# Kernel tuning notes

Measured on AMD Instinct MI355X. Metric: run time of the kernel, lower is better.

## Reference

```python
import jax, jax.numpy as jnp
import numpy as np

N = 50000
NEG_SLOPE = 0.2  # PyG GATConv default negative_slope


def gat_conv(x, src, dst, W, a_src, a_dst, b, num_nodes):
    """PyG-style GATConv (concat=True, add_self_loops handled by caller).
    x: [N, Fin], src/dst: [E'] (self-loops included), W: [Fin, H*C],
    a_src/a_dst: [H, C], b: [H*C].
    """
    H, C = a_src.shape
    h = (x @ W).reshape(num_nodes, H, C)                      # [N, H, C]
    alpha_src = jnp.einsum('nhc,hc->nh', h, a_src)            # [N, H]
    alpha_dst = jnp.einsum('nhc,hc->nh', h, a_dst)            # [N, H]
    e = jax.nn.leaky_relu(alpha_src[src] + alpha_dst[dst], NEG_SLOPE)  # [E', H]
    # segment softmax over edges grouped by destination node
    m = jax.ops.segment_max(e, dst, num_segments=num_nodes)   # [N, H]
    m = jnp.where(jnp.isfinite(m), m, 0.0)
    ex = jnp.exp(e - m[dst])                                  # [E', H]
    denom = jax.ops.segment_sum(ex, dst, num_segments=num_nodes)
    alpha = ex / (denom[dst] + 1e-16)                          # [E', H]
    # weighted scatter-sum of source features to destinations
    out = jax.ops.segment_sum(alpha[:, :, None] * h[src], dst, num_segments=num_nodes)
    return out.reshape(num_nodes, H * C) + b


def setup_inputs() -> dict:
    key = jax.random.key(0)
    ks = jax.random.split(key, 10)
    Fin, Hid, Out, Hds = 128, 32, 64, 4
    E = 800000
    x = jax.random.normal(ks[0], (N, Fin), dtype=jnp.float32)
    edge_index = jax.random.randint(ks[1], (2, E), 0, N, dtype=jnp.int64)
    s1 = (1.0 / np.sqrt(Fin)).astype(np.float32) if isinstance(np.sqrt(Fin), np.ndarray) else np.float32(1.0 / np.sqrt(Fin))
    s2 = np.float32(1.0 / np.sqrt(Hid * Hds))
    return {
        'x': x,
        'edge_index': edge_index,
        'W1': jax.random.normal(ks[2], (Fin, Hds * Hid), dtype=jnp.float32) * s1,
        'att_src1': jax.random.normal(ks[3], (Hds, Hid), dtype=jnp.float32) * 0.1,
        'att_dst1': jax.random.normal(ks[4], (Hds, Hid), dtype=jnp.float32) * 0.1,
        'b1': jnp.zeros((Hds * Hid,), dtype=jnp.float32),
        'W2': jax.random.normal(ks[5], (Hds * Hid, Out), dtype=jnp.float32) * s2,
        'att_src2': jax.random.normal(ks[6], (1, Out), dtype=jnp.float32) * 0.1,
        'att_dst2': jax.random.normal(ks[7], (1, Out), dtype=jnp.float32) * 0.1,
        'b2': jnp.zeros((Out,), dtype=jnp.float32),
    }


def reference(x, edge_index, W1, att_src1, att_dst1, b1, W2, att_src2, att_dst2, b2):
    num_nodes = x.shape[0]
    loop = jnp.arange(num_nodes, dtype=edge_index.dtype)
    src = jnp.concatenate([edge_index[0], loop])  # add self-loops (PyG default)
    dst = jnp.concatenate([edge_index[1], loop])
    h = gat_conv(x, src, dst, W1, att_src1, att_dst1, b1, num_nodes)
    h = jax.nn.relu(h)
    out = gat_conv(h, src, dst, W2, att_src2, att_dst2, b2, num_nodes)
    return out
```

## Files before the change

kernel.cpp:

```cpp
#include <hip/hip_runtime.h>
#include <hip/hip_fp16.h>

#define NN 50000
#define EE 800000
#define ELL (EE + NN)
#define NSLICE 8
#define SLICE_W (NN / NSLICE)
#define LCAP 131072
#define LCNT_STRIDE 16
#define BUCK_TILE 4096

__device__ __forceinline__ int edge_at(const void* ei, int is64, long long idx) {
  if (is64) return (int)((const long long*)ei)[idx];
  return ((const int*)ei)[idx];
}

__device__ __forceinline__ float leaky(float x) { return x > 0.f ? x : 0.2f * x; }


__global__ void __launch_bounds__(256) zero_detect_kernel(int* __restrict__ p, int n,
                                                          const unsigned* __restrict__ ei_words,
                                                          int* __restrict__ flag) {
  if (blockIdx.x == 0 && threadIdx.x == 0) {
    unsigned acc = 0;
    for (int i = 1; i < 64; i += 2) acc |= ei_words[i];
    *flag = (acc == 0u) ? 1 : 0;
  }
  int stride = gridDim.x * blockDim.x;
  for (int i = blockIdx.x * blockDim.x + threadIdx.x; i < n; i += stride) p[i] = 0;
}


__global__ void __launch_bounds__(256) bucket_kernel(const void* __restrict__ ei,
                                                     const int* __restrict__ flag,
                                                     unsigned* __restrict__ lists,
                                                     int* __restrict__ lcnt) {
  __shared__ int hist[NSLICE];
  __shared__ int base[NSLICE];
  __shared__ int cur[NSLICE];
  int is64 = *flag;
  int t = threadIdx.x;
  if (t < NSLICE) hist[t] = 0;
  __syncthreads();
  long long i0 = (long long)blockIdx.x * BUCK_TILE;
  unsigned pk[16];
  int sl[16];
  #pragma unroll
  for (int j = 0; j < 16; ++j) {
    long long i = i0 + t + j * 256;
    int s = -1, d = -1;
    if (i < EE) {
      s = edge_at(ei, is64, i);
      d = edge_at(ei, is64, (long long)EE + i);
    } else if (i < ELL) {
      s = d = (int)(i - EE);
    }
    if ((unsigned)s < (unsigned)NN && (unsigned)d < (unsigned)NN) {
      sl[j] = d / SLICE_W;
      pk[j] = (unsigned)s | ((unsigned)d << 16);
      atomicAdd(&hist[sl[j]], 1);
    } else {
      sl[j] = -1;
    }
  }
  __syncthreads();
  if (t < NSLICE) {
    base[t] = atomicAdd(&lcnt[t * LCNT_STRIDE], hist[t]);
    cur[t] = 0;
  }
  __syncthreads();
  #pragma unroll
  for (int j = 0; j < 16; ++j) {
    if (sl[j] >= 0) {
      int pos = base[sl[j]] + atomicAdd(&cur[sl[j]], 1);
      if (pos < LCAP) lists[(sl[j] << 17) + pos] = pk[j];
    }
  }
}


__global__ void __launch_bounds__(256) count_kernel(const unsigned* __restrict__ lists,
                                                    const int* __restrict__ lcnt,
                                                    int* __restrict__ cnt) {
  int fam = blockIdx.x & (NSLICE - 1);
  int bf = blockIdx.x >> 3;
  int nf = gridDim.x >> 3;
  int n = min(lcnt[fam * LCNT_STRIDE], LCAP);
  const unsigned* lp = lists + (fam << 17);
  for (int i = bf * blockDim.x + threadIdx.x; i < n; i += nf * blockDim.x)
    atomicAdd(&cnt[lp[i] >> 16], 1);
}

__global__ void __launch_bounds__(256) scan1_kernel(const int* __restrict__ cnt,
                                                    int* __restrict__ excl,
                                                    int* __restrict__ bsum) {
  __shared__ int sh[256];
  int t = threadIdx.x;
  int base = blockIdx.x * 1024 + t * 4;
  int v0 = 0, v1 = 0, v2 = 0, v3 = 0;
  if (base + 0 < NN) v0 = cnt[base + 0];
  if (base + 1 < NN) v1 = cnt[base + 1];
  if (base + 2 < NN) v2 = cnt[base + 2];
  if (base + 3 < NN) v3 = cnt[base + 3];
  int s = v0 + v1 + v2 + v3;
  sh[t] = s;
  __syncthreads();
  for (int off = 1; off < 256; off <<= 1) {
    int x = (t >= off) ? sh[t - off] : 0;
    __syncthreads();
    sh[t] += x;
    __syncthreads();
  }
  if (t == 255) bsum[blockIdx.x] = sh[255];
  int run = sh[t] - s;
  if (base + 0 < NN) excl[base + 0] = run;
  run += v0;
  if (base + 1 < NN) excl[base + 1] = run;
  run += v1;
  if (base + 2 < NN) excl[base + 2] = run;
  run += v2;
  if (base + 3 < NN) excl[base + 3] = run;
}

__global__ void scan2_kernel(int* __restrict__ bsum, int nb) {
  if (threadIdx.x == 0 && blockIdx.x == 0) {
    int run = 0;
    for (int i = 0; i < nb; ++i) { int x = bsum[i]; bsum[i] = run; run += x; }
    bsum[nb] = run;
  }
}

__global__ void __launch_bounds__(256) scan3_kernel(int* __restrict__ row_ptr,
                                                    const int* __restrict__ bsum,
                                                    int nb) {
  int i = blockIdx.x * blockDim.x + threadIdx.x;
  if (i < NN) row_ptr[i] += bsum[i >> 10];
  if (i == 0) row_ptr[NN] = bsum[nb];
}

__global__ void __launch_bounds__(256) scatter_kernel(const unsigned* __restrict__ lists,
                                                      const int* __restrict__ lcnt,
                                                      const int* __restrict__ row_ptr,
                                                      int* __restrict__ cursor,
                                                      unsigned* __restrict__ pairs) {
  int fam = blockIdx.x & (NSLICE - 1);
  int bf = blockIdx.x >> 3;
  int nf = gridDim.x >> 3;
  int n = min(lcnt[fam * LCNT_STRIDE], LCAP);
  const unsigned* lp = lists + (fam << 17);
  for (int i = bf * blockDim.x + threadIdx.x; i < n; i += nf * blockDim.x) {
    unsigned pk = lp[i];
    int d = pk >> 16;
    int pos = row_ptr[d] + atomicAdd(&cursor[d], 1);
    if ((unsigned)pos < (unsigned)ELL) pairs[pos] = pk;
  }
}


template <typename TA, int BM, int BN, int BK, int TM, int TN, int AMODE>
__global__ void __launch_bounds__(256) gemm_alpha(const TA* __restrict__ A,
                                                  const float* __restrict__ B,
                                                  __half* __restrict__ C,
                                                  const float* __restrict__ a_srcv,
                                                  const float* __restrict__ a_dstv,
                                                  float* __restrict__ asrc_out,
                                                  float* __restrict__ adst_out,
                                                  int M, int N, int K) {
  constexpr int THREADS = (BM / TM) * (BN / TN);
  static_assert(THREADS == 256, "block must be 256 threads");
  static_assert(BM * BK == 1024, "A tile = 4 elems/thread");
  static_assert((TN % 4) == 0 && (TM % 4) == 0, "microtile shape");
  constexpr int BPT = (BK * BN) / THREADS;
  static_assert(BPT == 2 || BPT == 4, "B tile load width");
  __shared__ float As[BK][BM + 4];
  __shared__ float Bs[BK][BN + 4];
  int tid = threadIdx.x;
  int tx = tid % (BN / TN);
  int ty = tid / (BN / TN);
  int row0 = blockIdx.x * BM;
  int col0 = blockIdx.y * BN;
  float acc[TM][TN] = {};
  for (int k0 = 0; k0 < K; k0 += BK) {
    {
      int m = tid / (BK / 4);
      int kk = (tid % (BK / 4)) * 4;
      int gr = row0 + m;
      float va[4] = {0.f, 0.f, 0.f, 0.f};
      if (gr < M) {
        if constexpr (sizeof(TA) == 4) {
          float4 v = *(const float4*)&A[(size_t)gr * K + k0 + kk];
          va[0] = v.x; va[1] = v.y; va[2] = v.z; va[3] = v.w;
        } else {
          uint2 raw = *(const uint2*)&A[(size_t)gr * K + k0 + kk];
          float2 f01 = __half22float2(__builtin_bit_cast(__half2, raw.x));
          float2 f23 = __half22float2(__builtin_bit_cast(__half2, raw.y));
          va[0] = f01.x; va[1] = f01.y; va[2] = f23.x; va[3] = f23.y;
        }
      }
      As[kk + 0][m] = va[0]; As[kk + 1][m] = va[1];
      As[kk + 2][m] = va[2]; As[kk + 3][m] = va[3];
    }
    if constexpr (BPT == 4) {
      constexpr int T_PER_ROW = BN / 4;
      int kr = tid / T_PER_ROW;
      int nc = (tid % T_PER_ROW) * 4;
      *(float4*)&Bs[kr][nc] = *(const float4*)&B[(size_t)(k0 + kr) * N + col0 + nc];
    } else {
      constexpr int T_PER_ROW = BN / 2;
      int kr = tid / T_PER_ROW;
      int nc = (tid % T_PER_ROW) * 2;
      *(float2*)&Bs[kr][nc] = *(const float2*)&B[(size_t)(k0 + kr) * N + col0 + nc];
    }
    __syncthreads();
    #pragma unroll
    for (int k = 0; k < BK; ++k) {
      float a[TM], b[TN];
      #pragma unroll
      for (int i = 0; i < TM; i += 4)
        *(float4*)&a[i] = *(const float4*)&As[k][ty * TM + i];
      #pragma unroll
      for (int j = 0; j < TN; j += 4)
        *(float4*)&b[j] = *(const float4*)&Bs[k][tx * TN + j];
      #pragma unroll
      for (int i = 0; i < TM; ++i)
        #pragma unroll
        for (int j = 0; j < TN; ++j) acc[i][j] += a[i] * b[j];
    }
    __syncthreads();
  }
  #pragma unroll
  for (int i = 0; i < TM; ++i) {
    int gr = row0 + ty * TM + i;
    if (gr >= M) continue;
    __half tmp[TN];
    #pragma unroll
    for (int j = 0; j < TN; ++j) tmp[j] = __float2half(acc[i][j]);
    if constexpr (TN == 8)
      *(float4*)&C[(size_t)gr * N + col0 + tx * TN] = *(float4*)tmp;
    else
      *(float2*)&C[(size_t)gr * N + col0 + tx * TN] = *(float2*)tmp;
  }
  if (AMODE == 1) {
    int hh = tx >> 2;
    int co = (tx & 3) * TN;
    #pragma unroll
    for (int i = 0; i < TM; ++i) {
      float sA = 0.f, sD = 0.f;
      #pragma unroll
      for (int j = 0; j < TN; ++j) {
        float v = acc[i][j];
        sA += v * a_srcv[hh * 32 + co + j];
        sD += v * a_dstv[hh * 32 + co + j];
      }
      sA += __shfl_xor(sA, 1, 64); sA += __shfl_xor(sA, 2, 64);
      sD += __shfl_xor(sD, 1, 64); sD += __shfl_xor(sD, 2, 64);
      int gr = row0 + ty * TM + i;
      if ((tx & 3) == 0 && gr < M) {
        asrc_out[gr * 4 + hh] = sA;
        adst_out[gr * 4 + hh] = sD;
      }
    }
  } else if (AMODE == 2) {
    #pragma unroll
    for (int i = 0; i < TM; ++i) {
      float sA = 0.f, sD = 0.f;
      #pragma unroll
      for (int j = 0; j < TN; ++j) {
        float v = acc[i][j];
        sA += v * a_srcv[tx * TN + j];
        sD += v * a_dstv[tx * TN + j];
      }
      #pragma unroll
      for (int m = 1; m <= 8; m <<= 1) {
        sA += __shfl_xor(sA, m, 64);
        sD += __shfl_xor(sD, m, 64);
      }
      int gr = row0 + ty * TM + i;
      if (tx == 0 && gr < M) { asrc_out[gr] = sA; adst_out[gr] = sD; }
    }
  }
}


__global__ void __launch_bounds__(256) agg1_fused(
    const __half* __restrict__ h,
    const int* __restrict__ row_ptr,
    const unsigned* __restrict__ pairs,
    const float* __restrict__ asrc,
    const float* __restrict__ adst,
    const float* __restrict__ b1,
    __half* __restrict__ out)
{
  int lane = threadIdx.x & 63;
  int grp = lane >> 5;
  int cl = lane & 31;
  int c0 = cl * 4;
  int myh = cl >> 3;
  int wid = (blockIdx.x * blockDim.x + threadIdx.x) >> 6;
  int nw = (gridDim.x * blockDim.x) >> 6;
  float4 bb = *(const float4*)&b1[c0];
  for (int n = wid; n < NN; n += nw) {
    int rbeg = row_ptr[n], rend = row_ptr[n + 1];
    float ad = adst[n * 4 + myh];
    float dsum = grp ? 0.f : 1e-16f;
    float a0 = 0.f, a1 = 0.f, a2 = 0.f, a3 = 0.f;
    #pragma unroll 8
    for (int e = rbeg + grp; e < rend; e += 2) {
      int s = pairs[e] & 0xFFFF;
      float wgt = __expf(leaky(asrc[s * 4 + myh] + ad));
      float2 raw = *(const float2*)&h[(size_t)s * 128 + c0];
      float2 f01 = __half22float2(__builtin_bit_cast(__half2, raw.x));
      float2 f23 = __half22float2(__builtin_bit_cast(__half2, raw.y));
      dsum += wgt;
      a0 += wgt * f01.x; a1 += wgt * f01.y;
      a2 += wgt * f23.x; a3 += wgt * f23.y;
    }
    dsum += __shfl_xor(dsum, 32, 64);
    a0 += __shfl_xor(a0, 32, 64);
    a1 += __shfl_xor(a1, 32, 64);
    a2 += __shfl_xor(a2, 32, 64);
    a3 += __shfl_xor(a3, 32, 64);
    if (lane < 32) {
      float inv = 1.f / dsum;
      __half ot[4];
      ot[0] = __float2half(fmaxf(a0 * inv + bb.x, 0.f));
      ot[1] = __float2half(fmaxf(a1 * inv + bb.y, 0.f));
      ot[2] = __float2half(fmaxf(a2 * inv + bb.z, 0.f));
      ot[3] = __float2half(fmaxf(a3 * inv + bb.w, 0.f));
      *(uint2*)&out[(size_t)n * 128 + c0] = *(uint2*)ot;
    }
  }
}

__global__ void __launch_bounds__(256) agg2_kernel(
    const __half* __restrict__ h,
    const int* __restrict__ row_ptr,
    const unsigned* __restrict__ pairs,
    const float* __restrict__ asrc,
    const float* __restrict__ adst,
    const float* __restrict__ b2,
    float* __restrict__ out)
{
  int lane = threadIdx.x & 63;
  int grp = lane >> 4;
  int cl = lane & 15;
  int c0 = cl * 4;
  int wid = (blockIdx.x * blockDim.x + threadIdx.x) >> 6;
  int nw = (gridDim.x * blockDim.x) >> 6;
  float4 bb = *(const float4*)&b2[c0];
  for (int n = wid; n < NN; n += nw) {
    int rbeg = row_ptr[n], rend = row_ptr[n + 1];
    float ad = adst[n];
    float dsum = (grp == 0) ? 1e-16f : 0.f;
    float a0 = 0.f, a1 = 0.f, a2 = 0.f, a3 = 0.f;
    #pragma unroll 4
    for (int e = rbeg + grp; e < rend; e += 4) {
      int s = pairs[e] & 0xFFFF;
      float wgt = __expf(leaky(asrc[s] + ad));
      float2 raw = *(const float2*)&h[(size_t)s * 64 + c0];
      float2 f01 = __half22float2(__builtin_bit_cast(__half2, raw.x));
      float2 f23 = __half22float2(__builtin_bit_cast(__half2, raw.y));
      dsum += wgt;
      a0 += wgt * f01.x; a1 += wgt * f01.y;
      a2 += wgt * f23.x; a3 += wgt * f23.y;
    }
    #pragma unroll
    for (int m = 16; m <= 32; m <<= 1) {
      dsum += __shfl_xor(dsum, m, 64);
      a0 += __shfl_xor(a0, m, 64);
      a1 += __shfl_xor(a1, m, 64);
      a2 += __shfl_xor(a2, m, 64);
      a3 += __shfl_xor(a3, m, 64);
    }
    if (lane < 16) {
      float inv = 1.f / dsum;
      float4 o = make_float4(a0 * inv + bb.x, a1 * inv + bb.y,
                             a2 * inv + bb.z, a3 * inv + bb.w);
      *(float4*)&out[(size_t)n * 64 + c0] = o;
    }
  }
}


extern "C" void kernel_launch(void* const* d_in, const int* in_sizes, int n_in,
                              void* d_out, int out_size, void* d_ws, size_t ws_size,
                              hipStream_t stream) {
  const float* x   = (const float*)d_in[0];
  const void*  ei  = d_in[1];
  const float* W1  = (const float*)d_in[2];
  const float* as1 = (const float*)d_in[3];
  const float* ad1 = (const float*)d_in[4];
  const float* b1  = (const float*)d_in[5];
  const float* W2  = (const float*)d_in[6];
  const float* as2 = (const float*)d_in[7];
  const float* ad2 = (const float*)d_in[8];
  const float* b2  = (const float*)d_in[9];
  float* out = (float*)d_out;

  char* w = (char*)d_ws;
  __half* h1h  = (__half*)w; w += (size_t)NN * 128 * 2;
  __half* hb2h = h1h;
  __half* h2   = (__half*)w; w += (size_t)NN * 128 * 2;
  float* asrc1 = (float*)w; w += (size_t)NN * 4 * 4;
  float* adst1 = (float*)w; w += (size_t)NN * 4 * 4;
  float* asrc2 = (float*)w; w += (size_t)NN * 4;
  float* adst2 = (float*)w; w += (size_t)NN * 4;
  int* cnt     = (int*)w;   w += (size_t)NN * 4;
  int* cursor  = (int*)w;   w += (size_t)NN * 4;
  int* lcnt    = (int*)w;   w += 512;
  int* row_ptr = (int*)w;   w += (size_t)(NN + 1) * 4;
  int* bsum    = (int*)w;   w += 256;
  int* is64    = (int*)w;   w += 256;
  unsigned* lists = (unsigned*)w; w += (size_t)NSLICE * LCAP * 4;
  unsigned* pairs = (unsigned*)w; w += (size_t)ELL * 4;

  const int NB = (NN + 1023) / 1024;
  const int MB128 = (NN + 127) / 128;
  const int BUCK_BLOCKS = (ELL + BUCK_TILE - 1) / BUCK_TILE;

  zero_detect_kernel<<<256, 256, 0, stream>>>(cnt, 2 * NN + 128, (const unsigned*)ei, is64);
  bucket_kernel<<<BUCK_BLOCKS, 256, 0, stream>>>(ei, is64, lists, lcnt);
  count_kernel<<<2048, 256, 0, stream>>>(lists, lcnt, cnt);
  scan1_kernel<<<NB, 256, 0, stream>>>(cnt, row_ptr, bsum);
  scan2_kernel<<<1, 64, 0, stream>>>(bsum, NB);
  scan3_kernel<<<(NN + 255) / 256, 256, 0, stream>>>(row_ptr, bsum, NB);

  gemm_alpha<float, 128, 128, 8, 8, 8, 1><<<dim3(MB128, 1), 256, 0, stream>>>(
      x, W1, h1h, as1, ad1, asrc1, adst1, NN, 128, 128);

  scatter_kernel<<<2048, 256, 0, stream>>>(lists, lcnt, row_ptr, cursor, pairs);

  agg1_fused<<<4096, 256, 0, stream>>>(h1h, row_ptr, pairs, asrc1, adst1, b1, h2);

  gemm_alpha<__half, 128, 64, 8, 8, 4, 2><<<dim3(MB128, 1), 256, 0, stream>>>(
      h2, W2, hb2h, as2, ad2, asrc2, adst2, NN, 64, 128);
  agg2_kernel<<<4096, 256, 0, stream>>>(hb2h, row_ptr, pairs, asrc2, adst2, b2, out);
}
```

Baseline: 231.2 us.

## Replace FP32 SIMT GEMMs with fp16 MFMA kernels fusing attention projections

```diff
diff --git a/kernel.cpp b/kernel.cpp
--- a/kernel.cpp
+++ b/kernel.cpp
@@ -9,6 +9,9 @@
 #define LCAP 131072
 #define LCNT_STRIDE 16
 #define BUCK_TILE 4096
+
+typedef _Float16 f16x8 __attribute__((ext_vector_type(8)));
+typedef float f32x4 __attribute__((ext_vector_type(4)));
 
 __device__ __forceinline__ int edge_at(const void* ei, int is64, long long idx) {
   if (is64) return (int)((const long long*)ei)[idx];
@@ -157,126 +160,131 @@
 }
 
 
-template <typename TA, int BM, int BN, int BK, int TM, int TN, int AMODE>
-__global__ void __launch_bounds__(256) gemm_alpha(const TA* __restrict__ A,
-                                                  const float* __restrict__ B,
-                                                  __half* __restrict__ C,
-                                                  const float* __restrict__ a_srcv,
-                                                  const float* __restrict__ a_dstv,
-                                                  float* __restrict__ asrc_out,
-                                                  float* __restrict__ adst_out,
-                                                  int M, int N, int K) {
-  constexpr int THREADS = (BM / TM) * (BN / TN);
-  static_assert(THREADS == 256, "block must be 256 threads");
-  static_assert(BM * BK == 1024, "A tile = 4 elems/thread");
-  static_assert((TN % 4) == 0 && (TM % 4) == 0, "microtile shape");
-  constexpr int BPT = (BK * BN) / THREADS;
-  static_assert(BPT == 2 || BPT == 4, "B tile load width");
-  __shared__ float As[BK][BM + 4];
-  __shared__ float Bs[BK][BN + 4];
-  int tid = threadIdx.x;
-  int tx = tid % (BN / TN);
-  int ty = tid / (BN / TN);
-  int row0 = blockIdx.x * BM;
-  int col0 = blockIdx.y * BN;
-  float acc[TM][TN] = {};
-  for (int k0 = 0; k0 < K; k0 += BK) {
-    {
-      int m = tid / (BK / 4);
-      int kk = (tid % (BK / 4)) * 4;
-      int gr = row0 + m;
-      float va[4] = {0.f, 0.f, 0.f, 0.f};
-      if (gr < M) {
-        if constexpr (sizeof(TA) == 4) {
-          float4 v = *(const float4*)&A[(size_t)gr * K + k0 + kk];
-          va[0] = v.x; va[1] = v.y; va[2] = v.z; va[3] = v.w;
-        } else {
-          uint2 raw = *(const uint2*)&A[(size_t)gr * K + k0 + kk];
-          float2 f01 = __half22float2(__builtin_bit_cast(__half2, raw.x));
-          float2 f23 = __half22float2(__builtin_bit_cast(__half2, raw.y));
-          va[0] = f01.x; va[1] = f01.y; va[2] = f23.x; va[3] = f23.y;
+template <int NT, int AMODE, typename TA>
+__global__ void __launch_bounds__(256) gemm_mfma(const TA* __restrict__ A,
+                                                 const float* __restrict__ B,
+                                                 __half* __restrict__ C,
+                                                 const float* __restrict__ a_srcv,
+                                                 const float* __restrict__ a_dstv,
+                                                 float* __restrict__ asrc_out,
+                                                 float* __restrict__ adst_out,
+                                                 int M) {
+  constexpr int NW = NT * 16;
+  __shared__ __align__(16) __half As[64][136];
+  __shared__ __align__(16) __half Bt[NW][136];
+  int t = threadIdx.x;
+  int row0 = blockIdx.x * 64;
+
+  if constexpr (sizeof(TA) == 4) {
+    #pragma unroll
+    for (int i = 0; i < 8; ++i) {
+      int idx = t + i * 256;
+      int row = idx >> 5, kq = idx & 31;
+      int gr = row0 + row;
+      float4 v = make_float4(0.f, 0.f, 0.f, 0.f);
+      if (gr < M) v = *(const float4*)&A[(size_t)gr * 128 + kq * 4];
+      __half h4[4] = {__float2half(v.x), __float2half(v.y),
+                      __float2half(v.z), __float2half(v.w)};
+      *(uint2*)&As[row][kq * 4] = *(uint2*)h4;
+    }
+  } else {
+    #pragma unroll
+    for (int i = 0; i < 4; ++i) {
+      int idx = t + i * 256;
+      int row = idx >> 4, kc = idx & 15;
+      int gr = row0 + row;
+      float4 raw = make_float4(0.f, 0.f, 0.f, 0.f);
+      if (gr < M) raw = *(const float4*)&A[(size_t)gr * 128 + kc * 8];
+      *(float4*)&As[row][kc * 8] = raw;
+    }
+  }
+  {
+    constexpr int HALF_N = NW / 2;
+    constexpr int ITER = 128 * HALF_N / 256;
+    #pragma unroll
+    for (int i = 0; i < ITER; ++i) {
+      int idx = t + i * 256;
+      int k = idx / HALF_N, n0 = (idx % HALF_N) * 2;
+      float2 v = *(const float2*)&B[(size_t)k * NW + n0];
+      Bt[n0][k] = __float2half(v.x);
+      Bt[n0 + 1][k] = __float2half(v.y);
+    }
+  }
+  __syncthreads();
+
+  int wv = t >> 6, l = t & 63;
+  int c = l & 15, rg = l >> 4;
+  f32x4 acc[NT];
+  #pragma unroll
+  for (int ct = 0; ct < NT; ++ct) acc[ct] = (f32x4){0.f, 0.f, 0.f, 0.f};
+
+  #pragma unroll
+  for (int ks = 0; ks < 4; ++ks) {
+    f16x8 af = *(const f16x8*)&As[wv * 16 + c][ks * 32 + rg * 8];
+    #pragma unroll
+    for (int ct = 0; ct < NT; ++ct) {
+      f16x8 bf = *(const f16x8*)&Bt[ct * 16 + c][ks * 32 + rg * 8];
+      acc[ct] = __builtin_amdgcn_mfma_f32_16x16x32_f16(af, bf, acc[ct], 0, 0, 0);
+    }
+  }
+
+  #pragma unroll
+  for (int r = 0; r < 4; ++r) {
+    int grow = row0 + wv * 16 + rg * 4 + r;
+    if (grow < M) {
+      #pragma unroll
+      for (int ct = 0; ct < NT; ++ct)
+        C[(size_t)grow * NW + ct * 16 + c] = __float2half(acc[ct][r]);
+    }
+  }
+
+  if constexpr (AMODE == 1) {
+    float aS[8], aD[8];
+    #pragma unroll
+    for (int h = 0; h < 4; ++h) {
+      aS[2 * h] = a_srcv[h * 32 + c];     aS[2 * h + 1] = a_srcv[h * 32 + 16 + c];
+      aD[2 * h] = a_dstv[h * 32 + c];     aD[2 * h + 1] = a_dstv[h * 32 + 16 + c];
+    }
+    #pragma unroll
+    for (int r = 0; r < 4; ++r) {
+      int grow = row0 + wv * 16 + rg * 4 + r;
+      #pragma unroll
+      for (int h = 0; h < 4; ++h) {
+        float s = acc[2 * h][r] * aS[2 * h] + acc[2 * h + 1][r] * aS[2 * h + 1];
+        float d = acc[2 * h][r] * aD[2 * h] + acc[2 * h + 1][r] * aD[2 * h + 1];
+        #pragma unroll
+        for (int m = 1; m <= 8; m <<= 1) {
+          s += __shfl_xor(s, m, 64);
+          d += __shfl_xor(d, m, 64);
+        }
+        if (c == 0 && grow < M) {
+          asrc_out[grow * 4 + h] = s;
+          adst_out[grow * 4 + h] = d;
         }
       }
-      As[kk + 0][m] = va[0]; As[kk + 1][m] = va[1];
-      As[kk + 2][m] = va[2]; As[kk + 3][m] = va[3];
-    }
-    if constexpr (BPT == 4) {
-      constexpr int T_PER_ROW = BN / 4;
-      int kr = tid / T_PER_ROW;
-      int nc = (tid % T_PER_ROW) * 4;
-      *(float4*)&Bs[kr][nc] = *(const float4*)&B[(size_t)(k0 + kr) * N + col0 + nc];
-    } else {
-      constexpr int T_PER_ROW = BN / 2;
-      int kr = tid / T_PER_ROW;
-      int nc = (tid % T_PER_ROW) * 2;
-      *(float2*)&Bs[kr][nc] = *(const float2*)&B[(size_t)(k0 + kr) * N + col0 + nc];
-    }
-    __syncthreads();
-    #pragma unroll
-    for (int k = 0; k < BK; ++k) {
-      float a[TM], b[TN];
+    }
+  } else {
+    float aS[NT], aD[NT];
+    #pragma unroll
+    for (int ct = 0; ct < NT; ++ct) {
+      aS[ct] = a_srcv[ct * 16 + c];
+      aD[ct] = a_dstv[ct * 16 + c];
+    }
+    #pragma unroll
+    for (int r = 0; r < 4; ++r) {
+      int grow = row0 + wv * 16 + rg * 4 + r;
+      float s = 0.f, d = 0.f;
       #pragma unroll
-      for (int i = 0; i < TM; i += 4)
-        *(float4*)&a[i] = *(const float4*)&As[k][ty * TM + i];
-      #pragma unroll
-      for (int j = 0; j < TN; j += 4)
-        *(float4*)&b[j] = *(const float4*)&Bs[k][tx * TN + j];
-      #pragma unroll
-      for (int i = 0; i < TM; ++i)
-        #pragma unroll
-        for (int j = 0; j < TN; ++j) acc[i][j] += a[i] * b[j];
-    }
-    __syncthreads();
-  }
-  #pragma unroll
-  for (int i = 0; i < TM; ++i) {
-    int gr = row0 + ty * TM + i;
-    if (gr >= M) continue;
-    __half tmp[TN];
-    #pragma unroll
-    for (int j = 0; j < TN; ++j) tmp[j] = __float2half(acc[i][j]);
-    if constexpr (TN == 8)
-      *(float4*)&C[(size_t)gr * N + col0 + tx * TN] = *(float4*)tmp;
-    else
-      *(float2*)&C[(size_t)gr * N + col0 + tx * TN] = *(float2*)tmp;
-  }
-  if (AMODE == 1) {
-    int hh = tx >> 2;
-    int co = (tx & 3) * TN;
-    #pragma unroll
-    for (int i = 0; i < TM; ++i) {
-      float sA = 0.f, sD = 0.f;
-      #pragma unroll
-      for (int j = 0; j < TN; ++j) {
-        float v = acc[i][j];
-        sA += v * a_srcv[hh * 32 + co + j];
-        sD += v * a_dstv[hh * 32 + co + j];
-      }
-      sA += __shfl_xor(sA, 1, 64); sA += __shfl_xor(sA, 2, 64);
-      sD += __shfl_xor(sD, 1, 64); sD += __shfl_xor(sD, 2, 64);
-      int gr = row0 + ty * TM + i;
-      if ((tx & 3) == 0 && gr < M) {
-        asrc_out[gr * 4 + hh] = sA;
-        adst_out[gr * 4 + hh] = sD;
-      }
-    }
-  } else if (AMODE == 2) {
-    #pragma unroll
-    for (int i = 0; i < TM; ++i) {
-      float sA = 0.f, sD = 0.f;
-      #pragma unroll
-      for (int j = 0; j < TN; ++j) {
-        float v = acc[i][j];
-        sA += v * a_srcv[tx * TN + j];
-        sD += v * a_dstv[tx * TN + j];
+      for (int ct = 0; ct < NT; ++ct) {
+        s += acc[ct][r] * aS[ct];
+        d += acc[ct][r] * aD[ct];
       }
       #pragma unroll
       for (int m = 1; m <= 8; m <<= 1) {
-        sA += __shfl_xor(sA, m, 64);
-        sD += __shfl_xor(sD, m, 64);
+        s += __shfl_xor(s, m, 64);
+        d += __shfl_xor(d, m, 64);
       }
-      int gr = row0 + ty * TM + i;
-      if (tx == 0 && gr < M) { asrc_out[gr] = sA; adst_out[gr] = sD; }
+      if (c == 0 && grow < M) { asrc_out[grow] = s; adst_out[grow] = d; }
     }
   }
 }
@@ -304,7 +312,7 @@
     float ad = adst[n * 4 + myh];
     float dsum = grp ? 0.f : 1e-16f;
     float a0 = 0.f, a1 = 0.f, a2 = 0.f, a3 = 0.f;
-    #pragma unroll 8
+    #pragma unroll 4
     for (int e = rbeg + grp; e < rend; e += 2) {
       int s = pairs[e] & 0xFFFF;
       float wgt = __expf(leaky(asrc[s * 4 + myh] + ad));
@@ -415,7 +423,7 @@
   unsigned* pairs = (unsigned*)w; w += (size_t)ELL * 4;
 
   const int NB = (NN + 1023) / 1024;
-  const int MB128 = (NN + 127) / 128;
+  const int MB64 = (NN + 63) / 64;
   const int BUCK_BLOCKS = (ELL + BUCK_TILE - 1) / BUCK_TILE;
 
   zero_detect_kernel<<<256, 256, 0, stream>>>(cnt, 2 * NN + 128, (const unsigned*)ei, is64);
@@ -425,14 +433,14 @@
   scan2_kernel<<<1, 64, 0, stream>>>(bsum, NB);
   scan3_kernel<<<(NN + 255) / 256, 256, 0, stream>>>(row_ptr, bsum, NB);
 
-  gemm_alpha<float, 128, 128, 8, 8, 8, 1><<<dim3(MB128, 1), 256, 0, stream>>>(
-      x, W1, h1h, as1, ad1, asrc1, adst1, NN, 128, 128);
+  gemm_mfma<8, 1, float><<<MB64, 256, 0, stream>>>(
+      x, W1, h1h, as1, ad1, asrc1, adst1, NN);
 
   scatter_kernel<<<2048, 256, 0, stream>>>(lists, lcnt, row_ptr, cursor, pairs);
 
   agg1_fused<<<4096, 256, 0, stream>>>(h1h, row_ptr, pairs, asrc1, adst1, b1, h2);
 
-  gemm_alpha<__half, 128, 64, 8, 8, 4, 2><<<dim3(MB128, 1), 256, 0, stream>>>(
-      h2, W2, hb2h, as2, ad2, asrc2, adst2, NN, 64, 128);
+  gemm_mfma<4, 2, __half><<<MB64, 256, 0, stream>>>(
+      h2, W2, hb2h, as2, ad2, asrc2, adst2, NN);
   agg2_kernel<<<4096, 256, 0, stream>>>(hb2h, row_ptr, pairs, asrc2, adst2, b2, out);
 }
```

Result: faster. 202.2 us (-12.6%).
